# Performance work log

Hardware: AMD Instinct MI355X
Metric: run time of the kernel (lower is better)

Reference implementation:

```python
import jax, jax.numpy as jnp
import numpy as np

NH, HD = 4, 16          # num_heads, head_dim (proj_dim = 64)
SCALE = HD ** -0.5
EPS = 1e-5
G = 16                  # GroupNorm groups = min(16, channels)


def _conv1x1(W, b, x):
    # 1x1 conv == channel-mixing matmul: W (out,in), x (B,in,H,W)
    return jnp.einsum('pc,bchw->bphw', W, x) + b[None, :, None, None]


def _attend(Wq, bq, Wk, bk, Wv, bv, Wo, bo, query, context):
    B, C, H, Wd = query.shape
    N = H * Wd
    q = _conv1x1(Wq, bq, query).astype(jnp.float32).reshape(B, NH, HD, N)
    k = _conv1x1(Wk, bk, context).astype(jnp.float32).reshape(B, NH, HD, N)
    v = _conv1x1(Wv, bv, context).astype(jnp.float32).reshape(B, NH, HD, N)
    attn = jax.nn.softmax(jnp.einsum('bhdn,bhdm->bhnm', q, k) * SCALE, axis=-1)
    out = jnp.einsum('bhdm,bhnm->bhdn', v, attn).reshape(B, NH * HD, H, Wd)
    return _conv1x1(Wo, bo, out)


def _gn(x, gamma, beta):
    B, C, H, W = x.shape
    xr = x.reshape(B, G, C // G, H, W)
    m = xr.mean(axis=(2, 3, 4), keepdims=True)
    v = xr.var(axis=(2, 3, 4), keepdims=True)
    xn = ((xr - m) * jax.lax.rsqrt(v + EPS)).reshape(B, C, H, W)
    return xn * gamma[None, :, None, None] + beta[None, :, None, None]


def setup_inputs() -> dict:
    key = jax.random.key(0)
    C, P, Bn, H, W = 256, 64, 2, 64, 64
    ks = iter(jax.random.split(key, 64))
    d = {}
    for m in ['a', 'b', 'c']:
        d[f'feat_{m}'] = jax.random.normal(next(ks), (Bn, C, H, W), jnp.float32)
    for m in ['a', 'b', 'c']:
        d[f'Wq_{m}'] = 0.02 * jax.random.normal(next(ks), (P, C), jnp.float32)
        d[f'bq_{m}'] = jnp.zeros((P,), jnp.float32)
        d[f'Wk_{m}'] = 0.02 * jax.random.normal(next(ks), (P, 2 * C), jnp.float32)
        d[f'bk_{m}'] = jnp.zeros((P,), jnp.float32)
        d[f'Wv_{m}'] = 0.02 * jax.random.normal(next(ks), (P, 2 * C), jnp.float32)
        d[f'bv_{m}'] = jnp.zeros((P,), jnp.float32)
        d[f'Wo_{m}'] = 0.02 * jax.random.normal(next(ks), (C, P), jnp.float32)
        d[f'bo_{m}'] = jnp.zeros((C,), jnp.float32)
        d[f'g_{m}'] = jnp.ones((C,), jnp.float32)
        d[f'be_{m}'] = jnp.zeros((C,), jnp.float32)
    return d


def reference(feat_a, feat_b, feat_c,
              Wq_a, bq_a, Wk_a, bk_a, Wv_a, bv_a, Wo_a, bo_a, g_a, be_a,
              Wq_b, bq_b, Wk_b, bk_b, Wv_b, bv_b, Wo_b, bo_b, g_b, be_b,
              Wq_c, bq_c, Wk_c, bk_c, Wv_c, bv_c, Wo_c, bo_c, g_c, be_c):
    bc = jnp.concatenate([feat_b, feat_c], axis=1)
    a_out = _gn(feat_a + _attend(Wq_a, bq_a, Wk_a, bk_a, Wv_a, bv_a, Wo_a, bo_a, feat_a, bc), g_a, be_a)
    ac = jnp.concatenate([feat_a, feat_c], axis=1)
    b_out = _gn(feat_b + _attend(Wq_b, bq_b, Wk_b, bk_b, Wv_b, bv_b, Wo_b, bo_b, feat_b, ac), g_b, be_b)
    ab = jnp.concatenate([feat_a, feat_b], axis=1)
    c_out = _gn(feat_c + _attend(Wq_c, bq_c, Wk_c, bk_c, Wv_c, bv_c, Wo_c, bo_c, feat_c, ab), g_c, be_c)
    return (a_out, b_out, c_out)
```

## Files before the change

kernel.cpp:

```cpp
#include <hip/hip_runtime.h>

#define B_ 2
#define C_ 256
#define P_ 64
#define N_ 4096
#define EPS_ 1e-5f
#define QSCALE_ 0.3606737602222409f

typedef _Float16 half2 __attribute__((ext_vector_type(2)));
typedef _Float16 half4 __attribute__((ext_vector_type(4)));
typedef _Float16 half8 __attribute__((ext_vector_type(8)));
typedef float f32x4 __attribute__((ext_vector_type(4)));

static __device__ __forceinline__ float fexp2(float x) {
  return __builtin_bit_cast(float, (int)fmaf(x, 8388608.0f, 1064872512.0f));
}

static __device__ __forceinline__ half2 pack2(float a, float b) {
  return __builtin_bit_cast(half2, __builtin_amdgcn_cvt_pkrtz(a, b));
}

struct TP {
  const float* feat[3];
  const float* Wq[3]; const float* bq[3];
  const float* Wk[3]; const float* bk[3];
  const float* Wv[3]; const float* bv[3];
  const float* Wo[3]; const float* bo[3];
  const float* gm[3]; const float* bt[3];
  _Float16* xT;
  _Float16* q16;
  _Float16* k16;
  _Float16* v16;
  _Float16* wq16[3];
  _Float16* wk16[3];
  _Float16* wv16[3];
  _Float16* wo16[3];
  float* stats;
  float* out;
  int ctx0[3]; int ctx1[3];
};

__global__ __launch_bounds__(256) void prep_kernel(TP P) {
  __shared__ _Float16 lt[64 * 72];
  const int m = blockIdx.z, b = blockIdx.y;
  const int tid = threadIdx.x;
  const int cblk = blockIdx.x >> 6, nblk = blockIdx.x & 63;
  {
    const int n = nblk * 64 + (tid & 63);
    const int cb = (tid >> 6) * 16;
    const float* __restrict__ in =
        P.feat[m] + (size_t)b * C_ * N_ + (size_t)(cblk * 64 + cb) * N_ + n;
    float f[16];
#pragma unroll
    for (int i = 0; i < 16; ++i) f[i] = in[(size_t)i * N_];
    half8 h0, h1;
#pragma unroll
    for (int j = 0; j < 8; ++j) { h0[j] = (_Float16)f[j]; h1[j] = (_Float16)f[8 + j]; }
    *(half8*)(lt + (tid & 63) * 72 + cb) = h0;
    *(half8*)(lt + (tid & 63) * 72 + cb + 8) = h1;
  }
  __syncthreads();
  {
    const int nr = tid >> 2, cs = (tid & 3) * 16;
    const half8 o0 = *(const half8*)(lt + nr * 72 + cs);
    const half8 o1 = *(const half8*)(lt + nr * 72 + cs + 8);
    _Float16* o = P.xT + ((size_t)(m * 2 + b) * N_ + nblk * 64 + nr) * C_ +
                  cblk * 64 + cs;
    *(half8*)o = o0;
    *(half8*)(o + 8) = o1;
  }
  if (b == 0 && blockIdx.x < 8) {
    const int s = blockIdx.x;
    const float* srcs[4] = {P.Wq[m], P.Wk[m], P.Wv[m], P.Wo[m]};
    _Float16* dsts[4] = {P.wq16[m], P.wk16[m], P.wv16[m], P.wo16[m]};
    const int sizes[4] = {64 * 256, 64 * 512, 64 * 512, 256 * 64};
#pragma unroll
    for (int a = 0; a < 4; ++a) {
      const int lo = sizes[a] / 8 * s, hi = sizes[a] / 8 * (s + 1);
      for (int i = lo + tid * 4; i < hi; i += 1024) {
        const float4 x = *(const float4*)(srcs[a] + i);
        half4 h; h[0] = (_Float16)x.x; h[1] = (_Float16)x.y;
        h[2] = (_Float16)x.z; h[3] = (_Float16)x.w;
        *(half4*)(dsts[a] + i) = h;
      }
    }
  }
  if (m == 0 && b == 0 && blockIdx.x == 8 && tid < 192) P.stats[tid] = 0.f;
}

#define PBS_ 264

__global__ __launch_bounds__(256) void proj_qkv_kernel(TP P) {
  __shared__ _Float16 bs[2 * 32 * PBS_];
  const int m = blockIdx.z, b = blockIdx.y;
  const int tid = threadIdx.x;
  const int w = tid >> 6, g = (tid >> 4) & 3, t = tid & 15;
  const bool is_q = blockIdx.x >= 128;
  const int n0 = (is_q ? blockIdx.x - 128 : (int)blockIdx.x) * 32;
  const int sr = tid >> 3, sc = (tid & 7) * 32;

  if (is_q) {
    const _Float16* __restrict__ xb =
        P.xT + ((size_t)(m * 2 + b) * N_ + n0 + sr) * C_ + sc;
#pragma unroll
    for (int j = 0; j < 4; ++j)
      *(half8*)(bs + sr * PBS_ + sc + j * 8) = *(const half8*)(xb + j * 8);
    __syncthreads();
    f32x4 a0 = {0.f,0.f,0.f,0.f}, a1 = {0.f,0.f,0.f,0.f};
#pragma unroll
    for (int ks = 0; ks < 8; ++ks) {
      const half8 a = *(const half8*)(P.wq16[m] + (w * 16 + t) * 256 + ks * 32 + g * 8);
      const half8 b0 = *(const half8*)(bs + t * PBS_ + ks * 32 + g * 8);
      const half8 b1 = *(const half8*)(bs + (16 + t) * PBS_ + ks * 32 + g * 8);
      a0 = __builtin_amdgcn_mfma_f32_16x16x32_f16(a, b0, a0, 0, 0, 0);
      a1 = __builtin_amdgcn_mfma_f32_16x16x32_f16(a, b1, a1, 0, 0, 0);
    }
    _Float16* qo = P.q16 + ((size_t)(m * 2 + b) * N_) * 64 + w * 16 + g * 4;
    half4 h0, h1;
#pragma unroll
    for (int r = 0; r < 4; ++r) {
      const float bq = P.bq[m][w * 16 + g * 4 + r];
      h0[r] = (_Float16)((a0[r] + bq) * QSCALE_);
      h1[r] = (_Float16)((a1[r] + bq) * QSCALE_);
    }
    *(half4*)(qo + (size_t)(n0 + t) * 64) = h0;
    *(half4*)(qo + (size_t)(n0 + 16 + t) * 64) = h1;
  } else {
    const int srcs[2] = {P.ctx0[m], P.ctx1[m]};
#pragma unroll
    for (int src = 0; src < 2; ++src) {
      const _Float16* __restrict__ xb =
          P.xT + ((size_t)(srcs[src] * 2 + b) * N_ + n0 + sr) * C_ + sc;
#pragma unroll
      for (int j = 0; j < 4; ++j)
        *(half8*)(bs + src * 32 * PBS_ + sr * PBS_ + sc + j * 8) =
            *(const half8*)(xb + j * 8);
    }
    __syncthreads();
    f32x4 k0 = {0.f,0.f,0.f,0.f}, k1 = {0.f,0.f,0.f,0.f};
    f32x4 v0 = {0.f,0.f,0.f,0.f}, v1 = {0.f,0.f,0.f,0.f};
#pragma unroll
    for (int src = 0; src < 2; ++src) {
#pragma unroll
      for (int ks = 0; ks < 8; ++ks) {
        const half8 ak = *(const half8*)(P.wk16[m] + (w * 16 + t) * 512 +
                                         src * 256 + ks * 32 + g * 8);
        const half8 av = *(const half8*)(P.wv16[m] + (w * 16 + t) * 512 +
                                         src * 256 + ks * 32 + g * 8);
        const half8 b0 = *(const half8*)(bs + src * 32 * PBS_ + t * PBS_ + ks * 32 + g * 8);
        const half8 b1 = *(const half8*)(bs + src * 32 * PBS_ + (16 + t) * PBS_ + ks * 32 + g * 8);
        k0 = __builtin_amdgcn_mfma_f32_16x16x32_f16(ak, b0, k0, 0, 0, 0);
        k1 = __builtin_amdgcn_mfma_f32_16x16x32_f16(ak, b1, k1, 0, 0, 0);
        v0 = __builtin_amdgcn_mfma_f32_16x16x32_f16(av, b0, v0, 0, 0, 0);
        v1 = __builtin_amdgcn_mfma_f32_16x16x32_f16(av, b1, v1, 0, 0, 0);
      }
    }
    const int bh = m * 8 + b * 4 + w;
    _Float16* ko = P.k16 + ((size_t)bh * N_) * 16 + g * 4;
    half4 h0, h1;
#pragma unroll
    for (int r = 0; r < 4; ++r) {
      const float bk = P.bk[m][w * 16 + g * 4 + r];
      h0[r] = (_Float16)(k0[r] + bk);
      h1[r] = (_Float16)(k1[r] + bk);
    }
    *(half4*)(ko + (size_t)(n0 + t) * 16) = h0;
    *(half4*)(ko + (size_t)(n0 + 16 + t) * 16) = h1;
    __syncthreads();
    _Float16* vt = bs;
#pragma unroll
    for (int r = 0; r < 4; ++r) {
      const float bv = P.bv[m][w * 16 + g * 4 + r];
      vt[(w * 16 + g * 4 + r) * 40 + t] = (_Float16)(v0[r] + bv);
      vt[(w * 16 + g * 4 + r) * 40 + 16 + t] = (_Float16)(v1[r] + bv);
    }
    __syncthreads();
    const int hh = tid >> 6, dd = (tid >> 2) & 15, nb = (tid & 3) * 8;
    const half8 hv8 = *(const half8*)(vt + (hh * 16 + dd) * 40 + nb);
    *(half8*)(P.v16 + ((size_t)(m * 8 + b * 4 + hh) * 16 + dd) * N_ + n0 + nb) = hv8;
  }
}

__global__ __launch_bounds__(256) void attn_kernel(TP P) {
  const int m = blockIdx.z, bh = blockIdx.y;
  const int tid = threadIdx.x;
  const int w = tid >> 6, g = (tid >> 4) & 3, t = tid & 15;
  const _Float16* __restrict__ kh = P.k16 + ((size_t)(m * 8 + bh) * N_) * 16;
  const _Float16* __restrict__ vh = P.v16 + ((size_t)(m * 8 + bh) * 16) * N_;
  const int b = bh >> 2, h = bh & 3;
  _Float16* qh = P.q16 + ((size_t)(m * 2 + b) * N_) * 64 + h * 16 + g * 4;

  const int q0 = blockIdx.x * 64 + w * 16;
  const half4 qf = *(const half4*)(qh + (size_t)(q0 + t) * 64);

  __shared__ _Float16 ks[128 * 16];
  __shared__ _Float16 vs[16 * 128];

  const int kr = tid >> 1, kc8 = tid & 1;
  const int vr = tid >> 4, vc = tid & 15;
  const _Float16* kgp = kh + (size_t)kr * 16 + kc8 * 8;
  const _Float16* vgp = vh + (size_t)vr * N_ + vc * 8;
  _Float16* ksp = ks + kr * 16 + ((kc8 ^ (kr & 1)) << 3);
  _Float16* vsp = vs + vr * 128 + ((vc ^ vr) << 3);

  half8 kpre = *(const half8*)kgp;
  half8 vpre = *(const half8*)vgp;

  f32x4 lacc = {0.f, 0.f, 0.f, 0.f};
  f32x4 O0 = {0.f,0.f,0.f,0.f}, O1 = {0.f,0.f,0.f,0.f};

  for (int kv0 = 0; kv0 < N_; kv0 += 128) {
    *(half8*)ksp = kpre;
    *(half8*)vsp = vpre;
    __syncthreads();
    const int nxt = (kv0 + 128 < N_) ? kv0 + 128 : 0;
    kpre = *(const half8*)(kgp + (size_t)nxt * 16);
    vpre = *(const half8*)(vgp + nxt);
#pragma unroll
    for (int hc = 0; hc < 2; ++hc) {
      f32x4 s[4];
#pragma unroll
      for (int i = 0; i < 4; ++i) {
        const int sub = hc * 4 + i;
        const half4 kf = *(const half4*)(ks + (sub * 16 + t) * 16 +
                          (((g >> 1) ^ (t & 1)) << 3) + (g & 1) * 4);
        const f32x4 z = {0.f, 0.f, 0.f, 0.f};
        s[i] = __builtin_amdgcn_mfma_f32_16x16x16f16(kf, qf, z, 0, 0, 0);
      }
      half4 pf[4];
#pragma unroll
      for (int i = 0; i < 4; ++i) {
        const float p0 = fexp2(s[i][0]), p1 = fexp2(s[i][1]);
        const float p2 = fexp2(s[i][2]), p3 = fexp2(s[i][3]);
        lacc[0] += p0; lacc[1] += p1; lacc[2] += p2; lacc[3] += p3;
        pf[i] = __builtin_shufflevector(pack2(p0, p1), pack2(p2, p3), 0, 1, 2, 3);
      }
#pragma unroll
      for (int i = 0; i < 4; ++i) {
        const int sub = hc * 4 + i;
        const half4 vf = *(const half4*)(vs + t * 128 +
                          (((sub * 2 + (g >> 1)) ^ t) << 3) + (g & 1) * 4);
        if (i & 1) O1 = __builtin_amdgcn_mfma_f32_16x16x16f16(vf, pf[i], O1, 0, 0, 0);
        else       O0 = __builtin_amdgcn_mfma_f32_16x16x16f16(vf, pf[i], O0, 0, 0, 0);
      }
    }
    __syncthreads();
  }
  float l = lacc[0] + lacc[1] + lacc[2] + lacc[3];
  l += __shfl_xor(l, 16);
  l += __shfl_xor(l, 32);
  const float inv = 1.0f / l;
  half4 hv;
#pragma unroll
  for (int r = 0; r < 4; ++r) hv[r] = (_Float16)((O0[r] + O1[r]) * inv);
  *(half4*)(qh + (size_t)(q0 + t) * 64) = hv;
}

#define BS_ 72

__global__ __launch_bounds__(256) void wo_resid_kernel(TP P) {
  __shared__ _Float16 as[64 * BS_];
  const int m = blockIdx.z;
  const int b = blockIdx.y >> 2, cblk = blockIdx.y & 3;
  const int n0 = blockIdx.x * 64;
  const int tid = threadIdx.x;
  const int w = tid >> 6, g = (tid >> 4) & 3, t = tid & 15;
  const int c0 = cblk * 64 + w * 16;
  const _Float16* __restrict__ ao = P.q16 + ((size_t)(m * 2 + b) * N_) * 64;
  const int ar = tid >> 2, ac = (tid & 3) * 16;
  const half8 l0 = *(const half8*)(ao + (size_t)(n0 + ar) * 64 + ac);
  const half8 l1 = *(const half8*)(ao + (size_t)(n0 + ar) * 64 + ac + 8);
  *(half8*)(as + ar * BS_ + ac) = l0;
  *(half8*)(as + ar * BS_ + ac + 8) = l1;
  __syncthreads();
  f32x4 acc[4] = {{0.f,0.f,0.f,0.f},{0.f,0.f,0.f,0.f},{0.f,0.f,0.f,0.f},{0.f,0.f,0.f,0.f}};
#pragma unroll
  for (int kst = 0; kst < 2; ++kst) {
    const half8 a =
        *(const half8*)(P.wo16[m] + (c0 + t) * 64 + kst * 32 + g * 8);
#pragma unroll
    for (int i = 0; i < 4; ++i) {
      const half8 bf = *(const half8*)(as + (i * 16 + t) * BS_ + kst * 32 + g * 8);
      acc[i] = __builtin_amdgcn_mfma_f32_16x16x32_f16(a, bf, acc[i], 0, 0, 0);
    }
  }
  const float* __restrict__ X = P.feat[m] + (size_t)b * C_ * N_;
  float* outb = P.out + (size_t)m * B_ * C_ * N_ + (size_t)b * C_ * N_;
  float s = 0.f, s2 = 0.f;
#pragma unroll
  for (int i = 0; i < 4; ++i) {
    const int n = n0 + i * 16 + t;
#pragma unroll
    for (int r = 0; r < 4; ++r) {
      const int c = c0 + g * 4 + r;
      const float val = acc[i][r] + X[(size_t)c * N_ + n] + P.bo[m][c];
      outb[(size_t)c * N_ + n] = val;
      s += val;
      s2 += val * val;
    }
  }
#pragma unroll
  for (int off = 1; off < 64; off <<= 1) {
    s += __shfl_xor(s, off);
    s2 += __shfl_xor(s2, off);
  }
  if ((tid & 63) == 0) {
    const int group = cblk * 4 + w;
    float* st = P.stats + ((size_t)(m * 2 + b) * 16 + group) * 2;
    atomicAdd(st, s);
    atomicAdd(st + 1, s2);
  }
}

__global__ __launch_bounds__(256) void gn_final_kernel(TP P) {
  const size_t base = ((size_t)blockIdx.x * 256 + threadIdx.x) * 4;
#pragma unroll
  for (int it = 0; it < 4; ++it) {
    const size_t idx = base + (size_t)it * 1572864;
    const int m = (int)(idx >> 21);
    const int rem = (int)(idx & ((1u << 21) - 1));
    const int b = rem >> 20;
    const int c = (rem >> 12) & 255;
    const float* st = P.stats + ((size_t)(m * 2 + b) * 16 + (c >> 4)) * 2;
    const float mean = st[0] * (1.f / 65536.f);
    const float var = st[1] * (1.f / 65536.f) - mean * mean;
    const float rstd = rsqrtf(var + EPS_);
    const float ga = P.gm[m][c] * rstd, be = P.bt[m][c];
    float4 x = *(float4*)(P.out + idx);
    x.x = (x.x - mean) * ga + be;
    x.y = (x.y - mean) * ga + be;
    x.z = (x.z - mean) * ga + be;
    x.w = (x.w - mean) * ga + be;
    *(float4*)(P.out + idx) = x;
  }
}

extern "C" void kernel_launch(void* const* d_in, const int* in_sizes, int n_in,
                              void* d_out, int out_size, void* d_ws, size_t ws_size,
                              hipStream_t stream) {
  TP P;
  for (int m = 0; m < 3; ++m) {
    P.feat[m] = (const float*)d_in[m];
    const int base = 3 + m * 10;
    P.Wq[m] = (const float*)d_in[base + 0];
    P.bq[m] = (const float*)d_in[base + 1];
    P.Wk[m] = (const float*)d_in[base + 2];
    P.bk[m] = (const float*)d_in[base + 3];
    P.Wv[m] = (const float*)d_in[base + 4];
    P.bv[m] = (const float*)d_in[base + 5];
    P.Wo[m] = (const float*)d_in[base + 6];
    P.bo[m] = (const float*)d_in[base + 7];
    P.gm[m] = (const float*)d_in[base + 8];
    P.bt[m] = (const float*)d_in[base + 9];
  }
  _Float16* ws = (_Float16*)d_ws;
  P.xT = ws;
  P.q16 = ws + 6291456;
  P.k16 = ws + 7864320;
  P.v16 = ws + 9437184;
  for (int m = 0; m < 3; ++m) {
    _Float16* wb = ws + 11010048 + (size_t)m * 98304;
    P.wq16[m] = wb;
    P.wk16[m] = wb + 16384;
    P.wv16[m] = wb + 49152;
    P.wo16[m] = wb + 81920;
  }
  P.stats = (float*)((char*)d_ws + 22609920);
  P.out = (float*)d_out;
  P.ctx0[0] = 1; P.ctx1[0] = 2;
  P.ctx0[1] = 0; P.ctx1[1] = 2;
  P.ctx0[2] = 0; P.ctx1[2] = 1;

  dim3 blk(256);
  prep_kernel<<<dim3(256, 2, 3), blk, 0, stream>>>(P);
  proj_qkv_kernel<<<dim3(256, 2, 3), blk, 0, stream>>>(P);
  attn_kernel<<<dim3(64, 8, 3), blk, 0, stream>>>(P);
  wo_resid_kernel<<<dim3(64, 8, 3), blk, 0, stream>>>(P);
  gn_final_kernel<<<dim3(1536), blk, 0, stream>>>(P);
}
```

Before: 281.7 us.

## Fuse fp16 prep into QKV projection and widen attention blocks

Removes the separate prep kernel. The projection kernel now reads fp32 features directly, transposes and converts them in shared memory, and converts fp32 weights to fp16 on the fly. This drops the xT and fp16 weight workspace round trip and one launch. The attention kernel moves to 512 threads with 128 queries and 256-key tiles per block, and stats zeroing moves into it. In exchange, each K/V projection block rereads strided fp32 features for both context sources and redoes the weight conversion per block.

```diff
diff --git a/kernel.cpp b/kernel.cpp
--- a/kernel.cpp
+++ b/kernel.cpp
@@ -7,17 +7,12 @@
 #define EPS_ 1e-5f
 #define QSCALE_ 0.3606737602222409f
 
-typedef _Float16 half2 __attribute__((ext_vector_type(2)));
 typedef _Float16 half4 __attribute__((ext_vector_type(4)));
 typedef _Float16 half8 __attribute__((ext_vector_type(8)));
 typedef float f32x4 __attribute__((ext_vector_type(4)));
 
 static __device__ __forceinline__ float fexp2(float x) {
   return __builtin_bit_cast(float, (int)fmaf(x, 8388608.0f, 1064872512.0f));
-}
-
-static __device__ __forceinline__ half2 pack2(float a, float b) {
-  return __builtin_bit_cast(half2, __builtin_amdgcn_cvt_pkrtz(a, b));
 }
 
 struct TP {
@@ -27,181 +22,168 @@
   const float* Wv[3]; const float* bv[3];
   const float* Wo[3]; const float* bo[3];
   const float* gm[3]; const float* bt[3];
-  _Float16* xT;
   _Float16* q16;
   _Float16* k16;
   _Float16* v16;
-  _Float16* wq16[3];
-  _Float16* wk16[3];
-  _Float16* wv16[3];
-  _Float16* wo16[3];
   float* stats;
   float* out;
   int ctx0[3]; int ctx1[3];
 };
 
-__global__ __launch_bounds__(256) void prep_kernel(TP P) {
-  __shared__ _Float16 lt[64 * 72];
-  const int m = blockIdx.z, b = blockIdx.y;
-  const int tid = threadIdx.x;
-  const int cblk = blockIdx.x >> 6, nblk = blockIdx.x & 63;
-  {
-    const int n = nblk * 64 + (tid & 63);
-    const int cb = (tid >> 6) * 16;
-    const float* __restrict__ in =
-        P.feat[m] + (size_t)b * C_ * N_ + (size_t)(cblk * 64 + cb) * N_ + n;
-    float f[16];
-#pragma unroll
-    for (int i = 0; i < 16; ++i) f[i] = in[(size_t)i * N_];
-    half8 h0, h1;
-#pragma unroll
-    for (int j = 0; j < 8; ++j) { h0[j] = (_Float16)f[j]; h1[j] = (_Float16)f[8 + j]; }
-    *(half8*)(lt + (tid & 63) * 72 + cb) = h0;
-    *(half8*)(lt + (tid & 63) * 72 + cb + 8) = h1;
-  }
-  __syncthreads();
-  {
-    const int nr = tid >> 2, cs = (tid & 3) * 16;
-    const half8 o0 = *(const half8*)(lt + nr * 72 + cs);
-    const half8 o1 = *(const half8*)(lt + nr * 72 + cs + 8);
-    _Float16* o = P.xT + ((size_t)(m * 2 + b) * N_ + nblk * 64 + nr) * C_ +
-                  cblk * 64 + cs;
-    *(half8*)o = o0;
-    *(half8*)(o + 8) = o1;
-  }
-  if (b == 0 && blockIdx.x < 8) {
-    const int s = blockIdx.x;
-    const float* srcs[4] = {P.Wq[m], P.Wk[m], P.Wv[m], P.Wo[m]};
-    _Float16* dsts[4] = {P.wq16[m], P.wk16[m], P.wv16[m], P.wo16[m]};
-    const int sizes[4] = {64 * 256, 64 * 512, 64 * 512, 256 * 64};
-#pragma unroll
-    for (int a = 0; a < 4; ++a) {
-      const int lo = sizes[a] / 8 * s, hi = sizes[a] / 8 * (s + 1);
-      for (int i = lo + tid * 4; i < hi; i += 1024) {
-        const float4 x = *(const float4*)(srcs[a] + i);
-        half4 h; h[0] = (_Float16)x.x; h[1] = (_Float16)x.y;
-        h[2] = (_Float16)x.z; h[3] = (_Float16)x.w;
-        *(half4*)(dsts[a] + i) = h;
-      }
-    }
-  }
-  if (m == 0 && b == 0 && blockIdx.x == 8 && tid < 192) P.stats[tid] = 0.f;
-}
-
-#define PBS_ 264
-
-__global__ __launch_bounds__(256) void proj_qkv_kernel(TP P) {
-  __shared__ _Float16 bs[2 * 32 * PBS_];
+#define PST_ 264
+#define VTS_ 88
+
+__global__ __launch_bounds__(256) void proj_fused_kernel(TP P) {
+  __shared__ _Float16 bs[64 * PST_];
   const int m = blockIdx.z, b = blockIdx.y;
   const int tid = threadIdx.x;
   const int w = tid >> 6, g = (tid >> 4) & 3, t = tid & 15;
-  const bool is_q = blockIdx.x >= 128;
-  const int n0 = (is_q ? blockIdx.x - 128 : (int)blockIdx.x) * 32;
-  const int sr = tid >> 3, sc = (tid & 7) * 32;
+  const bool is_q = blockIdx.x >= 64;
+  const int n0 = (is_q ? blockIdx.x - 64 : (int)blockIdx.x) * 64;
+  const int sn = tid & 63, scb = (tid >> 6) * 16;
 
   if (is_q) {
-    const _Float16* __restrict__ xb =
-        P.xT + ((size_t)(m * 2 + b) * N_ + n0 + sr) * C_ + sc;
-#pragma unroll
-    for (int j = 0; j < 4; ++j)
-      *(half8*)(bs + sr * PBS_ + sc + j * 8) = *(const half8*)(xb + j * 8);
-    __syncthreads();
-    f32x4 a0 = {0.f,0.f,0.f,0.f}, a1 = {0.f,0.f,0.f,0.f};
+    const float* __restrict__ in = P.feat[m] + (size_t)b * C_ * N_ + n0 + sn;
+#pragma unroll
+    for (int cc = 0; cc < 4; ++cc) {
+      const int c0 = cc * 64 + scb;
+      float f[16];
+#pragma unroll
+      for (int i = 0; i < 16; ++i) f[i] = in[(size_t)(c0 + i) * N_];
+      half8 h0, h1;
+#pragma unroll
+      for (int j = 0; j < 8; ++j) { h0[j] = (_Float16)f[j]; h1[j] = (_Float16)f[8 + j]; }
+      *(half8*)(bs + sn * PST_ + c0) = h0;
+      *(half8*)(bs + sn * PST_ + c0 + 8) = h1;
+    }
+    __syncthreads();
+    f32x4 a[4] = {{0.f,0.f,0.f,0.f},{0.f,0.f,0.f,0.f},{0.f,0.f,0.f,0.f},{0.f,0.f,0.f,0.f}};
+    const float* __restrict__ Wq = P.Wq[m] + (w * 16 + t) * 256;
 #pragma unroll
     for (int ks = 0; ks < 8; ++ks) {
-      const half8 a = *(const half8*)(P.wq16[m] + (w * 16 + t) * 256 + ks * 32 + g * 8);
-      const half8 b0 = *(const half8*)(bs + t * PBS_ + ks * 32 + g * 8);
-      const half8 b1 = *(const half8*)(bs + (16 + t) * PBS_ + ks * 32 + g * 8);
-      a0 = __builtin_amdgcn_mfma_f32_16x16x32_f16(a, b0, a0, 0, 0, 0);
-      a1 = __builtin_amdgcn_mfma_f32_16x16x32_f16(a, b1, a1, 0, 0, 0);
-    }
+      const float4 wa = *(const float4*)(Wq + ks * 32 + g * 8);
+      const float4 wb = *(const float4*)(Wq + ks * 32 + g * 8 + 4);
+      half8 af;
+      af[0] = (_Float16)wa.x; af[1] = (_Float16)wa.y;
+      af[2] = (_Float16)wa.z; af[3] = (_Float16)wa.w;
+      af[4] = (_Float16)wb.x; af[5] = (_Float16)wb.y;
+      af[6] = (_Float16)wb.z; af[7] = (_Float16)wb.w;
+#pragma unroll
+      for (int i = 0; i < 4; ++i) {
+        const half8 bf = *(const half8*)(bs + (i * 16 + t) * PST_ + ks * 32 + g * 8);
+        a[i] = __builtin_amdgcn_mfma_f32_16x16x32_f16(af, bf, a[i], 0, 0, 0);
+      }
+    }
+    float bq[4];
+#pragma unroll
+    for (int r = 0; r < 4; ++r) bq[r] = P.bq[m][w * 16 + g * 4 + r];
     _Float16* qo = P.q16 + ((size_t)(m * 2 + b) * N_) * 64 + w * 16 + g * 4;
-    half4 h0, h1;
+#pragma unroll
+    for (int i = 0; i < 4; ++i) {
+      half4 hq;
+#pragma unroll
+      for (int r = 0; r < 4; ++r) hq[r] = (_Float16)((a[i][r] + bq[r]) * QSCALE_);
+      *(half4*)(qo + (size_t)(n0 + i * 16 + t) * 64) = hq;
+    }
+  } else {
+    f32x4 ka[4] = {{0.f,0.f,0.f,0.f},{0.f,0.f,0.f,0.f},{0.f,0.f,0.f,0.f},{0.f,0.f,0.f,0.f}};
+    f32x4 va[4] = {{0.f,0.f,0.f,0.f},{0.f,0.f,0.f,0.f},{0.f,0.f,0.f,0.f},{0.f,0.f,0.f,0.f}};
+    const int srcs[2] = {P.ctx0[m], P.ctx1[m]};
+    for (int src = 0; src < 2; ++src) {
+      const float* __restrict__ in =
+          P.feat[srcs[src]] + (size_t)b * C_ * N_ + n0 + sn;
+      if (src) __syncthreads();
+#pragma unroll
+      for (int cc = 0; cc < 4; ++cc) {
+        const int c0 = cc * 64 + scb;
+        float f[16];
+#pragma unroll
+        for (int i = 0; i < 16; ++i) f[i] = in[(size_t)(c0 + i) * N_];
+        half8 h0, h1;
+#pragma unroll
+        for (int j = 0; j < 8; ++j) { h0[j] = (_Float16)f[j]; h1[j] = (_Float16)f[8 + j]; }
+        *(half8*)(bs + sn * PST_ + c0) = h0;
+        *(half8*)(bs + sn * PST_ + c0 + 8) = h1;
+      }
+      __syncthreads();
+      const float* __restrict__ Wk = P.Wk[m] + (w * 16 + t) * 512 + src * 256;
+      const float* __restrict__ Wv = P.Wv[m] + (w * 16 + t) * 512 + src * 256;
+#pragma unroll
+      for (int ks = 0; ks < 8; ++ks) {
+        const float4 k0 = *(const float4*)(Wk + ks * 32 + g * 8);
+        const float4 k1 = *(const float4*)(Wk + ks * 32 + g * 8 + 4);
+        const float4 v0 = *(const float4*)(Wv + ks * 32 + g * 8);
+        const float4 v1 = *(const float4*)(Wv + ks * 32 + g * 8 + 4);
+        half8 ak, av;
+        ak[0] = (_Float16)k0.x; ak[1] = (_Float16)k0.y;
+        ak[2] = (_Float16)k0.z; ak[3] = (_Float16)k0.w;
+        ak[4] = (_Float16)k1.x; ak[5] = (_Float16)k1.y;
+        ak[6] = (_Float16)k1.z; ak[7] = (_Float16)k1.w;
+        av[0] = (_Float16)v0.x; av[1] = (_Float16)v0.y;
+        av[2] = (_Float16)v0.z; av[3] = (_Float16)v0.w;
+        av[4] = (_Float16)v1.x; av[5] = (_Float16)v1.y;
+        av[6] = (_Float16)v1.z; av[7] = (_Float16)v1.w;
+#pragma unroll
+        for (int i = 0; i < 4; ++i) {
+          const half8 bf = *(const half8*)(bs + (i * 16 + t) * PST_ + ks * 32 + g * 8);
+          ka[i] = __builtin_amdgcn_mfma_f32_16x16x32_f16(ak, bf, ka[i], 0, 0, 0);
+          va[i] = __builtin_amdgcn_mfma_f32_16x16x32_f16(av, bf, va[i], 0, 0, 0);
+        }
+      }
+    }
+    float bk[4], bv[4];
 #pragma unroll
     for (int r = 0; r < 4; ++r) {
-      const float bq = P.bq[m][w * 16 + g * 4 + r];
-      h0[r] = (_Float16)((a0[r] + bq) * QSCALE_);
-      h1[r] = (_Float16)((a1[r] + bq) * QSCALE_);
-    }
-    *(half4*)(qo + (size_t)(n0 + t) * 64) = h0;
-    *(half4*)(qo + (size_t)(n0 + 16 + t) * 64) = h1;
-  } else {
-    const int srcs[2] = {P.ctx0[m], P.ctx1[m]};
-#pragma unroll
-    for (int src = 0; src < 2; ++src) {
-      const _Float16* __restrict__ xb =
-          P.xT + ((size_t)(srcs[src] * 2 + b) * N_ + n0 + sr) * C_ + sc;
-#pragma unroll
-      for (int j = 0; j < 4; ++j)
-        *(half8*)(bs + src * 32 * PBS_ + sr * PBS_ + sc + j * 8) =
-            *(const half8*)(xb + j * 8);
-    }
-    __syncthreads();
-    f32x4 k0 = {0.f,0.f,0.f,0.f}, k1 = {0.f,0.f,0.f,0.f};
-    f32x4 v0 = {0.f,0.f,0.f,0.f}, v1 = {0.f,0.f,0.f,0.f};
-#pragma unroll
-    for (int src = 0; src < 2; ++src) {
-#pragma unroll
-      for (int ks = 0; ks < 8; ++ks) {
-        const half8 ak = *(const half8*)(P.wk16[m] + (w * 16 + t) * 512 +
-                                         src * 256 + ks * 32 + g * 8);
-        const half8 av = *(const half8*)(P.wv16[m] + (w * 16 + t) * 512 +
-                                         src * 256 + ks * 32 + g * 8);
-        const half8 b0 = *(const half8*)(bs + src * 32 * PBS_ + t * PBS_ + ks * 32 + g * 8);
-        const half8 b1 = *(const half8*)(bs + src * 32 * PBS_ + (16 + t) * PBS_ + ks * 32 + g * 8);
-        k0 = __builtin_amdgcn_mfma_f32_16x16x32_f16(ak, b0, k0, 0, 0, 0);
-        k1 = __builtin_amdgcn_mfma_f32_16x16x32_f16(ak, b1, k1, 0, 0, 0);
-        v0 = __builtin_amdgcn_mfma_f32_16x16x32_f16(av, b0, v0, 0, 0, 0);
-        v1 = __builtin_amdgcn_mfma_f32_16x16x32_f16(av, b1, v1, 0, 0, 0);
-      }
-    }
-    const int bh = m * 8 + b * 4 + w;
-    _Float16* ko = P.k16 + ((size_t)bh * N_) * 16 + g * 4;
-    half4 h0, h1;
-#pragma unroll
-    for (int r = 0; r < 4; ++r) {
-      const float bk = P.bk[m][w * 16 + g * 4 + r];
-      h0[r] = (_Float16)(k0[r] + bk);
-      h1[r] = (_Float16)(k1[r] + bk);
-    }
-    *(half4*)(ko + (size_t)(n0 + t) * 16) = h0;
-    *(half4*)(ko + (size_t)(n0 + 16 + t) * 16) = h1;
-    __syncthreads();
-    _Float16* vt = bs;
-#pragma unroll
-    for (int r = 0; r < 4; ++r) {
-      const float bv = P.bv[m][w * 16 + g * 4 + r];
-      vt[(w * 16 + g * 4 + r) * 40 + t] = (_Float16)(v0[r] + bv);
-      vt[(w * 16 + g * 4 + r) * 40 + 16 + t] = (_Float16)(v1[r] + bv);
-    }
-    __syncthreads();
-    const int hh = tid >> 6, dd = (tid >> 2) & 15, nb = (tid & 3) * 8;
-    const half8 hv8 = *(const half8*)(vt + (hh * 16 + dd) * 40 + nb);
-    *(half8*)(P.v16 + ((size_t)(m * 8 + b * 4 + hh) * 16 + dd) * N_ + n0 + nb) = hv8;
-  }
-}
-
-__global__ __launch_bounds__(256) void attn_kernel(TP P) {
+      bk[r] = P.bk[m][w * 16 + g * 4 + r];
+      bv[r] = P.bv[m][w * 16 + g * 4 + r];
+    }
+    _Float16* ko = P.k16 + ((size_t)(m * 8 + b * 4 + w) * N_) * 16 + g * 4;
+#pragma unroll
+    for (int i = 0; i < 4; ++i) {
+      half4 hk;
+#pragma unroll
+      for (int r = 0; r < 4; ++r) hk[r] = (_Float16)(ka[i][r] + bk[r]);
+      *(half4*)(ko + (size_t)(n0 + i * 16 + t) * 16) = hk;
+    }
+    __syncthreads();
+#pragma unroll
+    for (int i = 0; i < 4; ++i)
+#pragma unroll
+      for (int r = 0; r < 4; ++r)
+        bs[(w * 16 + g * 4 + r) * VTS_ + i * 16 + t] = (_Float16)(va[i][r] + bv[r]);
+    __syncthreads();
+#pragma unroll
+    for (int pass = 0; pass < 2; ++pass) {
+      const int row = pass * 32 + (tid >> 3);
+      const int hh = row >> 4, dd = row & 15, nb = (tid & 7) * 8;
+      const half8 hv = *(const half8*)(bs + row * VTS_ + nb);
+      *(half8*)(P.v16 + ((size_t)(m * 8 + b * 4 + hh) * 16 + dd) * N_ + n0 + nb) = hv;
+    }
+  }
+}
+
+__global__ __launch_bounds__(512) void attn_kernel(TP P) {
   const int m = blockIdx.z, bh = blockIdx.y;
   const int tid = threadIdx.x;
+  if (m == 0 && bh == 0 && blockIdx.x == 0 && tid < 192) P.stats[tid] = 0.f;
   const int w = tid >> 6, g = (tid >> 4) & 3, t = tid & 15;
   const _Float16* __restrict__ kh = P.k16 + ((size_t)(m * 8 + bh) * N_) * 16;
   const _Float16* __restrict__ vh = P.v16 + ((size_t)(m * 8 + bh) * 16) * N_;
   const int b = bh >> 2, h = bh & 3;
   _Float16* qh = P.q16 + ((size_t)(m * 2 + b) * N_) * 64 + h * 16 + g * 4;
 
-  const int q0 = blockIdx.x * 64 + w * 16;
+  const int q0 = blockIdx.x * 128 + w * 16;
   const half4 qf = *(const half4*)(qh + (size_t)(q0 + t) * 64);
 
-  __shared__ _Float16 ks[128 * 16];
-  __shared__ _Float16 vs[16 * 128];
+  __shared__ _Float16 ks[256 * 16];
+  __shared__ _Float16 vs[16 * 256];
 
   const int kr = tid >> 1, kc8 = tid & 1;
-  const int vr = tid >> 4, vc = tid & 15;
+  const int vr = tid >> 5, vc = tid & 31;
   const _Float16* kgp = kh + (size_t)kr * 16 + kc8 * 8;
   const _Float16* vgp = vh + (size_t)vr * N_ + vc * 8;
   _Float16* ksp = ks + kr * 16 + ((kc8 ^ (kr & 1)) << 3);
-  _Float16* vsp = vs + vr * 128 + ((vc ^ vr) << 3);
+  _Float16* vsp = vs + vr * 256 + ((vc ^ vr) << 3);
 
   half8 kpre = *(const half8*)kgp;
   half8 vpre = *(const half8*)vgp;
@@ -209,15 +191,15 @@
   f32x4 lacc = {0.f, 0.f, 0.f, 0.f};
   f32x4 O0 = {0.f,0.f,0.f,0.f}, O1 = {0.f,0.f,0.f,0.f};
 
-  for (int kv0 = 0; kv0 < N_; kv0 += 128) {
+  for (int kv0 = 0; kv0 < N_; kv0 += 256) {
     *(half8*)ksp = kpre;
     *(half8*)vsp = vpre;
     __syncthreads();
-    const int nxt = (kv0 + 128 < N_) ? kv0 + 128 : 0;
+    const int nxt = (kv0 + 256 < N_) ? kv0 + 256 : 0;
     kpre = *(const half8*)(kgp + (size_t)nxt * 16);
     vpre = *(const half8*)(vgp + nxt);
 #pragma unroll
-    for (int hc = 0; hc < 2; ++hc) {
+    for (int hc = 0; hc < 4; ++hc) {
       f32x4 s[4];
 #pragma unroll
       for (int i = 0; i < 4; ++i) {
@@ -233,13 +215,13 @@
         const float p0 = fexp2(s[i][0]), p1 = fexp2(s[i][1]);
         const float p2 = fexp2(s[i][2]), p3 = fexp2(s[i][3]);
         lacc[0] += p0; lacc[1] += p1; lacc[2] += p2; lacc[3] += p3;
-        pf[i] = __builtin_shufflevector(pack2(p0, p1), pack2(p2, p3), 0, 1, 2, 3);
+        pf[i][0] = (_Float16)p0; pf[i][1] = (_Float16)p1;
+        pf[i][2] = (_Float16)p2; pf[i][3] = (_Float16)p3;
       }
 #pragma unroll
       for (int i = 0; i < 4; ++i) {
-        const int sub = hc * 4 + i;
-        const half4 vf = *(const half4*)(vs + t * 128 +
-                          (((sub * 2 + (g >> 1)) ^ t) << 3) + (g & 1) * 4);
+        const int c = (hc * 4 + i) * 2 + (g >> 1);
+        const half4 vf = *(const half4*)(vs + t * 256 + ((c ^ t) << 3) + (g & 1) * 4);
         if (i & 1) O1 = __builtin_amdgcn_mfma_f32_16x16x16f16(vf, pf[i], O1, 0, 0, 0);
         else       O0 = __builtin_amdgcn_mfma_f32_16x16x16f16(vf, pf[i], O0, 0, 0, 0);
       }
@@ -274,10 +256,16 @@
   *(half8*)(as + ar * BS_ + ac + 8) = l1;
   __syncthreads();
   f32x4 acc[4] = {{0.f,0.f,0.f,0.f},{0.f,0.f,0.f,0.f},{0.f,0.f,0.f,0.f},{0.f,0.f,0.f,0.f}};
+  const float* __restrict__ Wo = P.Wo[m] + (c0 + t) * 64;
 #pragma unroll
   for (int kst = 0; kst < 2; ++kst) {
-    const half8 a =
-        *(const half8*)(P.wo16[m] + (c0 + t) * 64 + kst * 32 + g * 8);
+    const float4 w0 = *(const float4*)(Wo + kst * 32 + g * 8);
+    const float4 w1 = *(const float4*)(Wo + kst * 32 + g * 8 + 4);
+    half8 a;
+    a[0] = (_Float16)w0.x; a[1] = (_Float16)w0.y;
+    a[2] = (_Float16)w0.z; a[3] = (_Float16)w0.w;
+    a[4] = (_Float16)w1.x; a[5] = (_Float16)w1.y;
+    a[6] = (_Float16)w1.z; a[7] = (_Float16)w1.w;
 #pragma unroll
     for (int i = 0; i < 4; ++i) {
       const half8 bf = *(const half8*)(as + (i * 16 + t) * BS_ + kst * 32 + g * 8);
@@ -354,27 +342,17 @@
     P.bt[m] = (const float*)d_in[base + 9];
   }
   _Float16* ws = (_Float16*)d_ws;
-  P.xT = ws;
-  P.q16 = ws + 6291456;
-  P.k16 = ws + 7864320;
-  P.v16 = ws + 9437184;
-  for (int m = 0; m < 3; ++m) {
-    _Float16* wb = ws + 11010048 + (size_t)m * 98304;
-    P.wq16[m] = wb;
-    P.wk16[m] = wb + 16384;
-    P.wv16[m] = wb + 49152;
-    P.wo16[m] = wb + 81920;
-  }
-  P.stats = (float*)((char*)d_ws + 22609920);
+  P.q16 = ws;
+  P.k16 = ws + 1572864;
+  P.v16 = ws + 3145728;
+  P.stats = (float*)(ws + 4718592);
   P.out = (float*)d_out;
   P.ctx0[0] = 1; P.ctx1[0] = 2;
   P.ctx0[1] = 0; P.ctx1[1] = 2;
   P.ctx0[2] = 0; P.ctx1[2] = 1;
 
-  dim3 blk(256);
-  prep_kernel<<<dim3(256, 2, 3), blk, 0, stream>>>(P);
-  proj_qkv_kernel<<<dim3(256, 2, 3), blk, 0, stream>>>(P);
-  attn_kernel<<<dim3(64, 8, 3), blk, 0, stream>>>(P);
-  wo_resid_kernel<<<dim3(64, 8, 3), blk, 0, stream>>>(P);
-  gn_final_kernel<<<dim3(1536), blk, 0, stream>>>(P);
-}
+  proj_fused_kernel<<<dim3(128, 2, 3), dim3(256), 0, stream>>>(P);
+  attn_kernel<<<dim3(32, 8, 3), dim3(512), 0, stream>>>(P);
+  wo_resid_kernel<<<dim3(64, 8, 3), dim3(256), 0, stream>>>(P);
+  gn_final_kernel<<<dim3(1536), dim3(256), 0, stream>>>(P);
+}
```

Measured after the change: 279.0 us. About the same (-1.0%).
